# Performance work log

Measured on AMD Instinct MI355X. Metric: run time of the kernel, lower is better.

The kernel has to match this reference:

```python
import jax, jax.numpy as jnp
import numpy as np

B, N, DIM = 4, 1024, 1024
H, DH, ORDER = 16, 64, 3
MAXREL = 64
INNER = H * DH
VOCAB = 2 * MAXREL + 1
SCALE = DH ** -0.5
TOPK = int(0.25 * N)  # topk_ratio=0.25 default when top_k is None


def setup_inputs() -> dict:
    key = jax.random.key(0)
    ks = jax.random.split(key, 8)
    s = 0.02
    return {
        "x": jax.random.normal(ks[0], (B, N, DIM), jnp.float32),
        "Wqkv": jax.random.normal(ks[1], (3 * INNER, DIM), jnp.float32) * s,
        "bqkv": jnp.zeros((3 * INNER,), jnp.float32),
        "Wout": jax.random.normal(ks[2], (DIM, INNER), jnp.float32) * s,
        "bout": jnp.zeros((DIM,), jnp.float32),
        "rel_k_emb": jax.random.normal(ks[3], (VOCAB, DH), jnp.float32) * s,
        "rel_v_emb": jax.random.normal(ks[4], (VOCAB, DH), jnp.float32) * s,
        "alphas_raw": jax.random.normal(ks[5], (ORDER, H), jnp.float32) * 0.5,
    }


def reference(x, Wqkv, bqkv, Wout, bout, rel_k_emb, rel_v_emb, alphas_raw):
    b, n, _ = x.shape
    qkv = x @ Wqkv.T + bqkv  # [b, n, 3*inner]
    q, k, v = jnp.split(qkv, 3, axis=-1)
    to_heads = lambda t: t.reshape(b, n, H, DH).transpose(0, 2, 1, 3)  # b h n d
    q, k, v = to_heads(q), to_heads(k), to_heads(v)

    scores = jnp.einsum('bhid,bhjd->bhij', q, k) * SCALE

    # relative position bias on keys
    coords = jnp.arange(n)
    dist = jnp.clip(coords[:, None] - coords[None, :], -MAXREL, MAXREL) + MAXREL  # [n, n]
    rel_k = rel_k_emb[dist]  # [n, n, d]
    scores = scores + jnp.einsum('bhid,ijd->bhij', q, rel_k)

    # top-k thresholding per query row
    top_vals = jax.lax.top_k(scores, TOPK)[0]
    threshold = top_vals[..., -1:]
    scores = jnp.where(scores < threshold, -jnp.inf, scores)

    attn = jax.nn.softmax(scores, axis=-1)  # [b, h, n, n]

    rel_v = rel_v_emb[dist]  # [n, n, d]
    alphas = jax.nn.sigmoid(alphas_raw)  # [order, h]

    # monomial-basis polynomial filter: res = sum_i alpha_i * A^(i+1) V (+ relV term at i=0)
    res = jnp.zeros_like(v)
    v_curr = v
    for i in range(ORDER):
        a_v = jnp.einsum('bhij,bhjd->bhid', attn, v_curr)
        if i == 0:
            a_v = a_v + jnp.einsum('bhij,ijd->bhid', attn, rel_v)
        v_curr = a_v
        res = res + alphas[i][None, :, None, None] * v_curr

    out = res.transpose(0, 2, 1, 3).reshape(b, n, INNER)
    return out @ Wout.T + bout
```

## Files before the change

kernel.cpp:

```cpp
#include <hip/hip_runtime.h>

typedef unsigned short u16;
typedef unsigned int   u32;
typedef unsigned long long u64;
typedef __bf16 bf16x8 __attribute__((ext_vector_type(8)));
typedef float  floatx4 __attribute__((ext_vector_type(4)));

#define DEV static __device__ __forceinline__

DEV u16 f2bf(float f){ u32 x = __float_as_uint(f); return (u16)((x + 0x7fffu + ((x>>16)&1u)) >> 16); }
DEV float bf2f(u16 h){ return __uint_as_float(((u32)h)<<16); }
DEV u32 cvt_pk_bf16(float a, float b){ u32 r; asm("v_cvt_pk_bf16_f32 %0, %1, %2" : "=v"(r) : "v"(a), "v"(b)); return r; }

DEV void load_lds16(const u16* g, u16* l){
  __builtin_amdgcn_global_load_lds((const __attribute__((address_space(1))) u32*)g,
                                   (__attribute__((address_space(3))) u32*)l, 16, 0, 0);
}

template<int BM, int BN, int MODE>
__global__ __launch_bounds__(256) void gemm_bt(
    const u16* __restrict__ A, const u16* __restrict__ Bm, float* __restrict__ C,
    const float* __restrict__ bias, int K, int lda, int ldb, int ldc, int ncmax,
    long long sA, long long sB, long long sC,
    u16* __restrict__ vout, float* __restrict__ resb, const float* __restrict__ araw,
    int order, int accum)
{
  constexpr int BK = 32;
  constexpr int MT = BM/32;
  constexpr int NT = (BN/2)/16;
  __shared__ u16 smem[8704];
  u16* As = smem;
  u16* Bs = smem + BM*BK;

  const int tid = threadIdx.x, wid = tid>>6, lane = tid&63;
  const int z = blockIdx.z;
  const int m0 = blockIdx.y * BM, n0 = blockIdx.x * BN;
  const u16* Ab = A + (long long)z*sA;
  const u16* Bb = Bm + (long long)z*sB;

  const int srow = tid>>2, schunk = (tid&3)*8;
  const u16* ga0 = Ab + (long long)(m0 + srow)*lda + schunk;
  const u16* gb0 = Bb + (long long)(n0 + srow)*ldb + schunk;
  const u16* ga1 = (BM==128) ? Ab + (long long)(m0 + 64 + srow)*lda + schunk : nullptr;
  const u16* gb1 = (BN==128) ? Bb + (long long)(n0 + 64 + srow)*ldb + schunk : nullptr;

  u16* lA0 = As + (wid*16)*BK;
  u16* lA1 = As + (64 + wid*16)*BK;
  u16* lB0 = Bs + (wid*16)*BK;
  u16* lB1 = Bs + (64 + wid*16)*BK;

  const int wm = wid>>1, wn = wid&1;
  const int lr = lane&15, lk = (lane>>4)*8, lq = lane>>4;

  floatx4 acc[MT][NT] = {};

  for (int k = 0; k < K; k += BK) {
    __syncthreads();
    load_lds16(ga0 + k, lA0);
    if constexpr (BM == 128) load_lds16(ga1 + k, lA1);
    load_lds16(gb0 + k, lB0);
    if constexpr (BN == 128) load_lds16(gb1 + k, lB1);
    __syncthreads();
    bf16x8 af[MT];
#pragma unroll
    for (int mt=0; mt<MT; ++mt)
      af[mt] = *(const bf16x8*)(As + (wm*(BM/2) + mt*16 + lr)*BK + lk);
#pragma unroll
    for (int nt=0; nt<NT; ++nt) {
      bf16x8 bfr = *(const bf16x8*)(Bs + (wn*(BN/2) + nt*16 + lr)*BK + lk);
#pragma unroll
      for (int mt=0; mt<MT; ++mt)
        acc[mt][nt] = __builtin_amdgcn_mfma_f32_16x16x32_bf16(af[mt], bfr, acc[mt][nt], 0, 0, 0);
    }
  }

  if constexpr (MODE == 0) {
    float* Cb = C + (long long)z*sC;
#pragma unroll
    for (int nt=0; nt<NT; ++nt) {
      const int col = n0 + wn*(BN/2) + nt*16 + lr;
      if (col < ncmax) {
        const float bv = bias ? bias[col] : 0.f;
#pragma unroll
        for (int mt=0; mt<MT; ++mt) {
#pragma unroll
          for (int r=0; r<4; ++r) {
            const int row = m0 + wm*(BM/2) + mt*16 + lq*4 + r;
            Cb[(long long)row*ldc + col] = acc[mt][nt][r] + bv;
          }
        }
      }
    }
  } else {
    const int h = z & 15;
    const float alpha = 1.f/(1.f + __expf(-araw[order*16 + h]));
    float* rb = resb + (long long)z * 65536;
    __syncthreads();
#pragma unroll
    for (int nt=0; nt<NT; ++nt) {
      const int d = wn*32 + nt*16 + lr;
#pragma unroll
      for (int mt=0; mt<MT; ++mt) {
#pragma unroll
        for (int r=0; r<4; ++r) {
          const int row = wm*(BM/2) + mt*16 + lq*4 + r;
          const float v = acc[mt][nt][r];
          const long long ri = (long long)(m0+row)*64 + d;
          rb[ri] = accum ? (rb[ri] + alpha*v) : (alpha*v);
          smem[d*136 + row] = f2bf(v);
        }
      }
    }
    __syncthreads();
    const int dd = tid>>2, cc = (tid&3)*(BM/4);
    u16* vp = vout + (long long)z*75776 + (long long)dd*1184 + m0 + cc;
    const u16* sp = smem + dd*136 + cc;
#pragma unroll
    for (int j=0; j<BM/4; j+=8) {
      uint4 uu;
      uu.x = sp[j+0] | ((u32)sp[j+1]<<16);
      uu.y = sp[j+2] | ((u32)sp[j+3]<<16);
      uu.z = sp[j+4] | ((u32)sp[j+5]<<16);
      uu.w = sp[j+6] | ((u32)sp[j+7]<<16);
      *(uint4*)(vp + j) = uu;
    }
  }
}

__global__ __launch_bounds__(1024, 8) void score_topk(
    const u16* __restrict__ qF,
    const u16* __restrict__ kxF,
    u16* __restrict__ P)
{
  constexpr int SROW = 1156;
  __shared__ float sm[16*SROW];
  const int tid = threadIdx.x, wid = tid>>6, lane = tid&63;
  const int L = blockIdx.x;
  const int z  = (L & 7) + ((L >> 9) << 3);
  const int mt = (L >> 3) & 63;
  const int m0 = mt*16;
  const int lr = lane&15, lq = lane>>4;

  const u16* Aq = qF + (((long long)z*64 + mt)*6*64 + lane)*8;
  const u16* Bq = kxF + ((long long)z*80*6*64 + lane)*8;

  bf16x8 af[6];
#pragma unroll
  for (int kc=0;kc<6;++kc) af[kc] = *(const bf16x8*)(Aq + kc*512);

  const int base = wid*5;
  {
    floatx4 acc[5];
#pragma unroll
    for (int t=0;t<5;++t) acc[t] = floatx4{0.f,0.f,0.f,0.f};
#pragma unroll
    for (int t=0;t<5;++t){
      if (base + t < 73){
        const u16* bp = Bq + (long long)(base+t)*3072;
        bf16x8 b0 = *(const bf16x8*)(bp);
        bf16x8 b1 = *(const bf16x8*)(bp + 512);
        bf16x8 b2 = *(const bf16x8*)(bp + 1024);
        bf16x8 b3 = *(const bf16x8*)(bp + 1536);
        bf16x8 b4 = *(const bf16x8*)(bp + 2048);
        bf16x8 b5 = *(const bf16x8*)(bp + 2560);
        acc[t] = __builtin_amdgcn_mfma_f32_16x16x32_bf16(af[0], b0, acc[t], 0, 0, 0);
        acc[t] = __builtin_amdgcn_mfma_f32_16x16x32_bf16(af[1], b1, acc[t], 0, 0, 0);
        acc[t] = __builtin_amdgcn_mfma_f32_16x16x32_bf16(af[2], b2, acc[t], 0, 0, 0);
        acc[t] = __builtin_amdgcn_mfma_f32_16x16x32_bf16(af[3], b3, acc[t], 0, 0, 0);
        acc[t] = __builtin_amdgcn_mfma_f32_16x16x32_bf16(af[4], b4, acc[t], 0, 0, 0);
        acc[t] = __builtin_amdgcn_mfma_f32_16x16x32_bf16(af[5], b5, acc[t], 0, 0, 0);
      }
    }
#pragma unroll
    for (int t=0;t<5;++t){
      if (base + t < 73){
        const int col = (base+t)*16 + lr;
        if (col < 1153){
#pragma unroll
          for (int r=0;r<4;++r) sm[(lq*4+r)*SROW + col] = acc[t][r];
        }
      }
    }
  }
  __syncthreads();

  {
    const int row = wid;
    const int i = m0 + row;
    float* R = sm + row*SROW;

    float v[16];
#pragma unroll
    for (int x=0;x<8;++x){
      float2 f = *(const float2*)(R + x*128 + lane*2);
      v[2*x] = f.x; v[2*x+1] = f.y;
    }
#pragma unroll
    for (int x=0;x<16;++x){
      const int j = (x>>1)*128 + lane*2 + (x&1);
      int dl = i - j; dl = dl > 64 ? 64 : (dl < -64 ? -64 : dl);
      v[x] += R[1024 + dl + 64];
    }
    u32 u[16];
#pragma unroll
    for (int x=0;x<16;++x){
      u32 bb = __float_as_uint(v[x]);
      u[x] = bb ^ ((u32)((int)bb >> 31) | 0x80000000u);
    }
    u32 thr = 0;
#pragma unroll 1
    for (int bit=31; bit>=0; --bit){
      const u32 cand = thr | (1u<<bit);
      int c = 0;
#pragma unroll
      for (int x=0;x<16;++x) c += __popcll(__ballot(u[x] >= cand));
      if (c == 256){
        u32 mn = 0xFFFFFFFFu;
#pragma unroll
        for (int x=0;x<16;++x) if (u[x] >= cand && u[x] < mn) mn = u[x];
        for (int o=32;o;o>>=1){ u32 t = __shfl_xor(mn, o); mn = t < mn ? t : mn; }
        thr = mn;
        break;
      }
      if (c > 256) thr = cand;
    }
    float m = -3.0e38f;
#pragma unroll
    for (int x=0;x<16;++x) m = fmaxf(m, v[x]);
    for (int o=32;o;o>>=1) m = fmaxf(m, __shfl_xor(m, o));
    float e[16]; float Z = 0.f;
#pragma unroll
    for (int x=0;x<16;++x){
      e[x] = (u[x] >= thr) ? __expf(v[x]-m) : 0.f;
      Z += e[x];
    }
    for (int o=32;o;o>>=1) Z += __shfl_xor(Z, o);
    const float rz = 1.f / Z;

    u16* Pr = P + ((long long)z*1024 + i)*1184;
    u32* Pr32 = (u32*)Pr;
    float s0 = 0.f, s1 = 0.f;
#pragma unroll
    for (int x=0;x<8;++x){
      const float p0 = e[2*x]*rz, p1 = e[2*x+1]*rz;
      *(float2*)(R + x*128 + lane*2) = float2{p0, p1};
      Pr32[x*64 + lane] = cvt_pk_bf16(p0, p1);
      const int j0 = x*128 + lane*2;
      if (j0     >= i+64) s0 += p0;
      if (j0     <= i-64) s1 += p0;
      if (j0 + 1 >= i+64) s0 += p1;
      if (j0 + 1 <= i-64) s1 += p1;
    }
    for (int o=32;o;o>>=1){ s0 += __shfl_xor(s0,o); s1 += __shfl_xor(s1,o); }
    {
      const int t = lane + 1;
      const int j = i + 64 - t;
      const float wv = (j>=0 && j<1024) ? R[j] : 0.f;
      Pr[1024 + t] = f2bf(wv);
      if (lane < 63){
        const int t2 = lane + 65;
        const int j2 = i + 64 - t2;
        const float wv2 = (j2>=0 && j2<1024) ? R[j2] : 0.f;
        Pr[1024 + t2] = f2bf(wv2);
      }
      if (lane == 0){ Pr[1024] = f2bf(s0); Pr[1152] = f2bf(s1); }
      if (lane >= 33) Pr[1120 + lane] = 0;
    }
  }
}

__global__ __launch_bounds__(256) void planeize(const float* __restrict__ src, u16* __restrict__ dst,
                                                int total, int modeB){
  int idx = blockIdx.x*256 + threadIdx.x;
  if (idx >= total) return;
  int c = idx & 1023, r = idx >> 10;
  float v = src[idx];
  u16 hi = f2bf(v); u16 lo = f2bf(v - bf2f(hi));
  u16* d = dst + (long long)r*3072 + c;
  if (modeB){ d[0]=hi; d[1024]=hi; d[2048]=lo; }
  else      { d[0]=hi; d[1024]=lo; d[2048]=hi; }
}

__global__ __launch_bounds__(256) void build_qk(const float* __restrict__ qkv,
                                                u16* __restrict__ qF, u16* __restrict__ kxF){
  int idx = blockIdx.x*256 + threadIdx.x;
  int d = idx & 63, n = (idx>>6) & 1023, bh = idx >> 16;
  int b = bh >> 4, h = bh & 15;
  long long src = (long long)(b*1024 + n)*3072 + h*64 + d;
  float qv = qkv[src];
  float kv = qkv[src + 1024] * 0.125f;
  u16 qhi=f2bf(qv), qlo=f2bf(qv - bf2f(qhi));
  u16 khi=f2bf(kv), klo=f2bf(kv - bf2f(khi));
  const int lane = (n&15) + (((d&31)>>3)<<4);
  const int elem = d&7, kc0 = d>>5;
  u16* q = qF + ((((long long)bh*64 + (n>>4))*6*64) + lane)*8 + elem;
  q[(kc0+0)*512] = qhi; q[(kc0+2)*512] = qlo; q[(kc0+4)*512] = qhi;
  u16* kx = kxF + ((((long long)bh*80 + (n>>4))*6*64) + lane)*8 + elem;
  kx[(kc0+0)*512] = khi; kx[(kc0+2)*512] = khi; kx[(kc0+4)*512] = klo;
}

__global__ __launch_bounds__(256) void build_kxrel(const float* __restrict__ relk, u16* __restrict__ kxF){
  int idx = blockIdx.x*256 + threadIdx.x;
  int d = idx & 63, t = (idx>>6) & 255, bh = idx >> 14;
  u16 hi=0, lo=0;
  if (t < 129){ float v = relk[t*64 + d]; hi = f2bf(v); lo = f2bf(v - bf2f(hi)); }
  const int nrow = 1024 + t;
  const int lane = (t&15) + (((d&31)>>3)<<4);
  const int elem = d&7, kc0 = d>>5;
  u16* kx = kxF + ((((long long)bh*80 + (nrow>>4))*6*64) + lane)*8 + elem;
  kx[(kc0+0)*512] = hi; kx[(kc0+2)*512] = hi; kx[(kc0+4)*512] = lo;
}

__global__ __launch_bounds__(256) void build_vT(const float* __restrict__ qkv, u16* __restrict__ vA){
  __shared__ float tb[64][65];
  int bh = blockIdx.x >> 4, ntile = blockIdx.x & 15;
  int b = bh >> 4, h = bh & 15;
  int tid = threadIdx.x;
  int nl = tid >> 2, dc = (tid & 3)*16;
  const float* sp = qkv + (long long)(b*1024 + ntile*64 + nl)*3072 + 2048 + h*64 + dc;
#pragma unroll
  for (int j=0;j<16;j+=4){
    float4 f = *(const float4*)(sp + j);
    tb[dc+j+0][nl]=f.x; tb[dc+j+1][nl]=f.y; tb[dc+j+2][nl]=f.z; tb[dc+j+3][nl]=f.w;
  }
  __syncthreads();
  int d = tid >> 2, nc = (tid & 3)*16;
  u16* dp = vA + ((long long)bh*64 + d)*1184 + ntile*64 + nc;
#pragma unroll
  for (int j=0;j<16;j+=8){
    u16 a0=f2bf(tb[d][nc+j+0]), a1=f2bf(tb[d][nc+j+1]), a2=f2bf(tb[d][nc+j+2]), a3=f2bf(tb[d][nc+j+3]);
    u16 a4=f2bf(tb[d][nc+j+4]), a5=f2bf(tb[d][nc+j+5]), a6=f2bf(tb[d][nc+j+6]), a7=f2bf(tb[d][nc+j+7]);
    uint4 uu; uu.x=a0|((u32)a1<<16); uu.y=a2|((u32)a3<<16); uu.z=a4|((u32)a5<<16); uu.w=a6|((u32)a7<<16);
    *(uint4*)(dp + j) = uu;
  }
}

__global__ __launch_bounds__(256) void build_vText(const float* __restrict__ relv, u16* __restrict__ vA){
  int idx = blockIdx.x*256 + threadIdx.x;
  int t = idx % 160; int rest = idx / 160; int d = rest & 63; int bh = rest >> 6;
  u16 hv = 0;
  if (t < 129) hv = f2bf(relv[t*64 + d]);
  vA[((long long)bh*64 + d)*1184 + 1024 + t] = hv;
}

__global__ __launch_bounds__(256) void build_resS(const float* __restrict__ res, u16* __restrict__ resS){
  int idx = blockIdx.x*256 + threadIdx.x;
  int d = idx & 63, n = (idx>>6) & 1023, bh = idx >> 16;
  int b = bh >> 4, h = bh & 15;
  float v = res[idx];
  u16 hi = f2bf(v), lo = f2bf(v - bf2f(hi));
  u16* p = resS + (long long)(b*1024 + n)*3072 + h*64 + d;
  p[0]=hi; p[1024]=lo; p[2048]=hi;
}

extern "C" void kernel_launch(void* const* d_in, const int* in_sizes, int n_in,
                              void* d_out, int out_size, void* d_ws, size_t ws_size,
                              hipStream_t stream) {
  const float* x    = (const float*)d_in[0];
  const float* Wqkv = (const float*)d_in[1];
  const float* bqkv = (const float*)d_in[2];
  const float* Wout = (const float*)d_in[3];
  const float* bout = (const float*)d_in[4];
  const float* relk = (const float*)d_in[5];
  const float* relv = (const float*)d_in[6];
  const float* araw = (const float*)d_in[7];
  float* out = (float*)d_out;

  char* w = (char*)d_ws;
  size_t off = 0;
  auto take = [&](size_t bytes)->char*{ char* p = w + off; off += (bytes + 255) & ~(size_t)255; return p; };

  char* regionA = take(94371840);
  u16*   xS    = (u16*)  (regionA);
  u16*   wqS   = (u16*)  (regionA + 25165824);
  float* qkv32 = (float*)(regionA + 44040192);
  u16*   Ph    = (u16*)  (regionA);
  u16*   resS  = (u16*)  (regionA);
  u16*   woS   = (u16*)  (regionA + 25165824);
  u16*   qF    = (u16*)take(25165824);
  u16*   kxF   = (u16*)take(31457280);
  u16*   vA    = (u16*)take(9699328);
  u16*   vB    = (u16*)take(9699328);
  float* res   = (float*)take(16777216);
  (void)ws_size; (void)in_sizes; (void)n_in; (void)out_size;

  planeize<<<16384,256,0,stream>>>(x,    xS,  4194304, 0);
  planeize<<<12288,256,0,stream>>>(Wqkv, wqS, 3145728, 1);
  gemm_bt<128,128,0><<<dim3(16,32,1),256,0,stream>>>(xS, wqS, qkv32, bqkv,
      3072, 3072, 3072, 3072, 2048, 0, 0, 0, nullptr, nullptr, nullptr, 0, 0);
  gemm_bt<128,128,0><<<dim3(8,32,1),256,0,stream>>>(xS, wqS + (long long)2048*3072,
      qkv32 + 2048, bqkv + 2048,
      1024, 3072, 3072, 3072, 1024, 0, 0, 0, nullptr, nullptr, nullptr, 0, 0);
  build_qk   <<<16384,256,0,stream>>>(qkv32, qF, kxF);
  build_kxrel<<<4096, 256,0,stream>>>(relk, kxF);
  build_vT   <<<1024, 256,0,stream>>>(qkv32, vA);
  build_vText<<<2560, 256,0,stream>>>(relv, vA);

  for (int half = 0; half < 2; ++half) {
    const long long zo = (long long)half * 32;
    score_topk<<<2048,1024,0,stream>>>(qF + zo*196608, kxF + zo*245760, Ph);
    gemm_bt<64,64,1><<<dim3(1,16,32),256,0,stream>>>(Ph, vA + zo*75776, nullptr, nullptr,
        1184, 1184, 1184, 0, 0, 1212416LL, 75776LL, 0LL,
        vB + zo*75776, res + zo*65536, araw, 0, 0);
    gemm_bt<64,64,1><<<dim3(1,16,32),256,0,stream>>>(Ph, vB + zo*75776, nullptr, nullptr,
        1024, 1184, 1184, 0, 0, 1212416LL, 75776LL, 0LL,
        vA + zo*75776, res + zo*65536, araw, 1, 1);
    gemm_bt<64,64,1><<<dim3(1,16,32),256,0,stream>>>(Ph, vA + zo*75776, nullptr, nullptr,
        1024, 1184, 1184, 0, 0, 1212416LL, 75776LL, 0LL,
        vB + zo*75776, res + zo*65536, araw, 2, 1);
  }

  build_resS<<<16384,256,0,stream>>>(res, resS);
  planeize  <<<4096, 256,0,stream>>>(Wout, woS, 1048576, 1);
  gemm_bt<64,128,0><<<dim3(8,64,1),256,0,stream>>>(resS, woS, out, bout,
      3072, 3072, 3072, 1024, 1024, 0, 0, 0, nullptr, nullptr, nullptr, 0, 0);
}
```

Measured before the change: 617.6 us.

## Swizzle GEMM LDS layout and add small-tile double-buffered AV kernel

Applies an XOR swizzle to the LDS tile layout in gemm_bt, with a matching permuted global-load mapping, to cut bank conflicts on fragment reads. It also replaces the 64x64 attention-times-V GEMM launches with a new av16 kernel that uses 16-row tiles, double-buffered LDS staging and 2048 blocks to raise occupancy and parallelism. The last hop skips writing V back since nothing reads it. The smaller tiles reload the V tile for every 16 query rows, trading data reuse for parallelism.

New measurement: 630.9 us. 2.2% more time.

```diff
diff --git a/kernel.cpp b/kernel.cpp
--- a/kernel.cpp
+++ b/kernel.cpp
@@ -15,6 +15,18 @@
 DEV void load_lds16(const u16* g, u16* l){
   __builtin_amdgcn_global_load_lds((const __attribute__((address_space(1))) u32*)g,
                                    (__attribute__((address_space(3))) u32*)l, 16, 0, 0);
+}
+
+DEV u32 unswz64(u32 p){
+  u32 r0 = ((p>>6) ^ (p>>8)) & 1u;
+  u32 b4 = ((p>>4) & 1u) ^ r0;
+  u32 b5 = ((p>>5) ^ (p>>7)) & 1u;
+  return (p & ~0x70u) | (b4<<4) | (b5<<5) | (r0<<6);
+}
+DEV bf16x8 ldfrag(const u16* base, int row, int lane){
+  u32 off = ((u32)row<<6) + (((u32)lane>>4)<<4);
+  off ^= (u32)(row&7)<<4;
+  return *(const bf16x8*)((const char*)base + off);
 }
 
 template<int BM, int BN, int MODE>
@@ -38,7 +50,8 @@
   const u16* Ab = A + (long long)z*sA;
   const u16* Bb = Bm + (long long)z*sB;
 
-  const int srow = tid>>2, schunk = (tid&3)*8;
+  const u32 g = unswz64((u32)tid*16);
+  const int srow = g>>6, schunk = (g&63)>>1;
   const u16* ga0 = Ab + (long long)(m0 + srow)*lda + schunk;
   const u16* gb0 = Bb + (long long)(n0 + srow)*ldb + schunk;
   const u16* ga1 = (BM==128) ? Ab + (long long)(m0 + 64 + srow)*lda + schunk : nullptr;
@@ -50,7 +63,7 @@
   u16* lB1 = Bs + (64 + wid*16)*BK;
 
   const int wm = wid>>1, wn = wid&1;
-  const int lr = lane&15, lk = (lane>>4)*8, lq = lane>>4;
+  const int lr = lane&15, lq = lane>>4;
 
   floatx4 acc[MT][NT] = {};
 
@@ -64,10 +77,10 @@
     bf16x8 af[MT];
 #pragma unroll
     for (int mt=0; mt<MT; ++mt)
-      af[mt] = *(const bf16x8*)(As + (wm*(BM/2) + mt*16 + lr)*BK + lk);
+      af[mt] = ldfrag(As, wm*(BM/2) + mt*16 + lr, lane);
 #pragma unroll
     for (int nt=0; nt<NT; ++nt) {
-      bf16x8 bfr = *(const bf16x8*)(Bs + (wn*(BN/2) + nt*16 + lr)*BK + lk);
+      bf16x8 bfr = ldfrag(Bs, wn*(BN/2) + nt*16 + lr, lane);
 #pragma unroll
       for (int mt=0; mt<MT; ++mt)
         acc[mt][nt] = __builtin_amdgcn_mfma_f32_16x16x32_bf16(af[mt], bfr, acc[mt][nt], 0, 0, 0);
@@ -124,6 +137,66 @@
       uu.w = sp[j+6] | ((u32)sp[j+7]<<16);
       *(uint4*)(vp + j) = uu;
     }
+  }
+}
+
+__global__ __launch_bounds__(256, 8) void av16(
+    const u16* __restrict__ P,
+    const u16* __restrict__ V,
+    u16* __restrict__ vout,
+    float* __restrict__ resb,
+    const float* __restrict__ araw, int K, int order, int accum, int wv)
+{
+  __shared__ u16 As[2][16*32];
+  __shared__ u16 Bs[2][64*32];
+  const int tid = threadIdx.x, wid = tid>>6, lane = tid&63;
+  const int L = blockIdx.x;
+  const int z = (L & 7) + ((L >> 9) << 3);
+  const int m0 = ((L >> 3) & 63) * 16;
+  const int lr = lane&15, lq = lane>>4;
+
+  const u32 ga = unswz64((u32)lane*16);
+  const int arow = ga>>6, acolu = (ga&63)>>1;
+  const u32 gb = unswz64((u32)tid*16);
+  const int brow = gb>>6, bcolu = (gb&63)>>1;
+  const u16* srcA = P + (long long)z*1212416 + (long long)(m0 + arow)*1184 + acolu;
+  const u16* srcB = V + (long long)z*75776  + (long long)brow*1184 + bcolu;
+
+  auto stage = [&](int buf, int k){
+    if (wid == 0) load_lds16(srcA + k, &As[buf][lane*8]);
+    load_lds16(srcB + k, &Bs[buf][tid*8]);
+  };
+
+  stage(0, 0);
+  __syncthreads();
+
+  floatx4 acc = {0.f,0.f,0.f,0.f};
+  const int nk = K >> 5;
+  for (int s = 0; s < nk; ++s){
+    const int cur = s & 1;
+    if (s + 1 < nk) stage(cur ^ 1, (s+1) << 5);
+    bf16x8 a = ldfrag(As[cur], lr, lane);
+    bf16x8 b = ldfrag(Bs[cur], wid*16 + lr, lane);
+    acc = __builtin_amdgcn_mfma_f32_16x16x32_bf16(a, b, acc, 0, 0, 0);
+    __syncthreads();
+  }
+
+  const int h = z & 15;
+  const float alpha = 1.f/(1.f + __expf(-araw[order*16 + h]));
+  const int d = wid*16 + lr;
+  float* rb = resb + (long long)z * 65536;
+  u32 w0, w1;
+#pragma unroll
+  for (int r=0; r<4; ++r){
+    const float v = acc[r];
+    const long long ri = (long long)(m0 + lq*4 + r)*64 + d;
+    rb[ri] = accum ? (rb[ri] + alpha*v) : (alpha*v);
+  }
+  if (wv){
+    w0 = f2bf(acc[0]) | ((u32)f2bf(acc[1])<<16);
+    w1 = f2bf(acc[2]) | ((u32)f2bf(acc[3])<<16);
+    u16* vp = vout + (long long)z*75776 + (long long)d*1184 + m0 + lq*4;
+    *(uint2*)vp = uint2{w0, w1};
   }
 }
 
@@ -399,15 +472,12 @@
   for (int half = 0; half < 2; ++half) {
     const long long zo = (long long)half * 32;
     score_topk<<<2048,1024,0,stream>>>(qF + zo*196608, kxF + zo*245760, Ph);
-    gemm_bt<64,64,1><<<dim3(1,16,32),256,0,stream>>>(Ph, vA + zo*75776, nullptr, nullptr,
-        1184, 1184, 1184, 0, 0, 1212416LL, 75776LL, 0LL,
-        vB + zo*75776, res + zo*65536, araw, 0, 0);
-    gemm_bt<64,64,1><<<dim3(1,16,32),256,0,stream>>>(Ph, vB + zo*75776, nullptr, nullptr,
-        1024, 1184, 1184, 0, 0, 1212416LL, 75776LL, 0LL,
-        vA + zo*75776, res + zo*65536, araw, 1, 1);
-    gemm_bt<64,64,1><<<dim3(1,16,32),256,0,stream>>>(Ph, vA + zo*75776, nullptr, nullptr,
-        1024, 1184, 1184, 0, 0, 1212416LL, 75776LL, 0LL,
-        vB + zo*75776, res + zo*65536, araw, 2, 1);
+    av16<<<2048,256,0,stream>>>(Ph, vA + zo*75776, vB + zo*75776, res + zo*65536,
+        araw, 1184, 0, 0, 1);
+    av16<<<2048,256,0,stream>>>(Ph, vB + zo*75776, vA + zo*75776, res + zo*65536,
+        araw, 1024, 1, 1, 1);
+    av16<<<2048,256,0,stream>>>(Ph, vA + zo*75776, vB + zo*75776, res + zo*65536,
+        araw, 1024, 2, 1, 0);
   }
 
   build_resS<<<16384,256,0,stream>>>(res, resS);
```

## Swizzle GEMM LDS tiles and use 8-wave kernel for projection GEMMs

Applied to the files above, without the earlier changes.

Adds an XOR swizzle to the LDS tile layout. The global source address of each lane's global_load_lds is permuted, and fragment reads apply the matching XOR, to cut LDS bank conflicts in the bf16 MFMA GEMMs. The batched P·V gemm_bt loses its 128-row second-load path, since it is now used only with 64x64 tiles. A new 512-thread, 8-wave gemm8 kernel replaces gemm_bt for the QKV and output projections, so each wave holds fewer accumulators and more waves share each staged tile. The risk is higher register and LDS pressure per block, and the swizzle math must stay consistent between the write and read sides.

Measured after the change: 596.4 us. 3.4% less time.

```diff
diff --git a/kernel.cpp b/kernel.cpp
--- a/kernel.cpp
+++ b/kernel.cpp
@@ -15,6 +15,18 @@
 DEV void load_lds16(const u16* g, u16* l){
   __builtin_amdgcn_global_load_lds((const __attribute__((address_space(1))) u32*)g,
                                    (__attribute__((address_space(3))) u32*)l, 16, 0, 0);
+}
+
+DEV u32 unswz64(u32 p){
+  u32 r0 = ((p>>6) ^ (p>>8)) & 1u;
+  u32 b4 = ((p>>4) & 1u) ^ r0;
+  u32 b5 = ((p>>5) ^ (p>>7)) & 1u;
+  return (p & ~0x70u) | (b4<<4) | (b5<<5) | (r0<<6);
+}
+DEV bf16x8 ldfrag(const u16* base, int row, int lane){
+  u32 off = ((u32)row<<6) + (((u32)lane>>4)<<4);
+  off ^= (u32)(row&7)<<4;
+  return *(const bf16x8*)((const char*)base + off);
 }
 
 template<int BM, int BN, int MODE>
@@ -38,36 +50,31 @@
   const u16* Ab = A + (long long)z*sA;
   const u16* Bb = Bm + (long long)z*sB;
 
-  const int srow = tid>>2, schunk = (tid&3)*8;
+  const u32 g = unswz64((u32)tid*16);
+  const int srow = g>>6, schunk = (g&63)>>1;
   const u16* ga0 = Ab + (long long)(m0 + srow)*lda + schunk;
   const u16* gb0 = Bb + (long long)(n0 + srow)*ldb + schunk;
-  const u16* ga1 = (BM==128) ? Ab + (long long)(m0 + 64 + srow)*lda + schunk : nullptr;
-  const u16* gb1 = (BN==128) ? Bb + (long long)(n0 + 64 + srow)*ldb + schunk : nullptr;
 
   u16* lA0 = As + (wid*16)*BK;
-  u16* lA1 = As + (64 + wid*16)*BK;
   u16* lB0 = Bs + (wid*16)*BK;
-  u16* lB1 = Bs + (64 + wid*16)*BK;
 
   const int wm = wid>>1, wn = wid&1;
-  const int lr = lane&15, lk = (lane>>4)*8, lq = lane>>4;
+  const int lr = lane&15, lq = lane>>4;
 
   floatx4 acc[MT][NT] = {};
 
   for (int k = 0; k < K; k += BK) {
     __syncthreads();
     load_lds16(ga0 + k, lA0);
-    if constexpr (BM == 128) load_lds16(ga1 + k, lA1);
     load_lds16(gb0 + k, lB0);
-    if constexpr (BN == 128) load_lds16(gb1 + k, lB1);
     __syncthreads();
     bf16x8 af[MT];
 #pragma unroll
     for (int mt=0; mt<MT; ++mt)
-      af[mt] = *(const bf16x8*)(As + (wm*(BM/2) + mt*16 + lr)*BK + lk);
+      af[mt] = ldfrag(As, wm*(BM/2) + mt*16 + lr, lane);
 #pragma unroll
     for (int nt=0; nt<NT; ++nt) {
-      bf16x8 bfr = *(const bf16x8*)(Bs + (wn*(BN/2) + nt*16 + lr)*BK + lk);
+      bf16x8 bfr = ldfrag(Bs, wn*(BN/2) + nt*16 + lr, lane);
 #pragma unroll
       for (int mt=0; mt<MT; ++mt)
         acc[mt][nt] = __builtin_amdgcn_mfma_f32_16x16x32_bf16(af[mt], bfr, acc[mt][nt], 0, 0, 0);
@@ -123,6 +130,67 @@
       uu.z = sp[j+4] | ((u32)sp[j+5]<<16);
       uu.w = sp[j+6] | ((u32)sp[j+7]<<16);
       *(uint4*)(vp + j) = uu;
+    }
+  }
+}
+
+template<int BM, int BN>
+__global__ __launch_bounds__(512, 4) void gemm8(
+    const u16* __restrict__ A, const u16* __restrict__ Bm, float* __restrict__ C,
+    const float* __restrict__ bias, int K, int lda, int ldb, int ldc, int ncmax)
+{
+  constexpr int MT = (BM/2)/16;
+  constexpr int NT = (BN/4)/16;
+  __shared__ u16 As[BM*32];
+  __shared__ u16 Bs[BN*32];
+
+  const int tid = threadIdx.x, wid = tid>>6, lane = tid&63;
+  const int m0 = blockIdx.y * BM, n0 = blockIdx.x * BN;
+
+  const u32 g = unswz64((u32)tid*16);
+  const int srow = g>>6, schunk = (g&63)>>1;
+  const u16* ga0 = A  + (long long)(m0 + srow)*lda + schunk;
+  const u16* gb0 = Bm + (long long)(n0 + srow)*ldb + schunk;
+
+  u16* lA = As + (wid<<9);
+  u16* lB = Bs + (wid<<9);
+
+  const int wm = wid>>2, wn = wid&3;
+  const int lr = lane&15, lq = lane>>4;
+
+  floatx4 acc[MT][NT] = {};
+
+  for (int k = 0; k < K; k += 32) {
+    __syncthreads();
+    if (BM == 128 || wid < 4) load_lds16(ga0 + k, lA);
+    load_lds16(gb0 + k, lB);
+    __syncthreads();
+    bf16x8 af[MT];
+#pragma unroll
+    for (int mt=0; mt<MT; ++mt)
+      af[mt] = ldfrag(As, wm*(BM/2) + mt*16 + lr, lane);
+#pragma unroll
+    for (int nt=0; nt<NT; ++nt) {
+      bf16x8 bfr = ldfrag(Bs, wn*(BN/4) + nt*16 + lr, lane);
+#pragma unroll
+      for (int mt=0; mt<MT; ++mt)
+        acc[mt][nt] = __builtin_amdgcn_mfma_f32_16x16x32_bf16(af[mt], bfr, acc[mt][nt], 0, 0, 0);
+    }
+  }
+
+#pragma unroll
+  for (int nt=0; nt<NT; ++nt) {
+    const int col = n0 + wn*(BN/4) + nt*16 + lr;
+    if (col < ncmax) {
+      const float bv = bias ? bias[col] : 0.f;
+#pragma unroll
+      for (int mt=0; mt<MT; ++mt) {
+#pragma unroll
+        for (int r=0; r<4; ++r) {
+          const int row = m0 + wm*(BM/2) + mt*16 + lq*4 + r;
+          C[(long long)row*ldc + col] = acc[mt][nt][r] + bv;
+        }
+      }
     }
   }
 }
@@ -386,11 +454,10 @@
 
   planeize<<<16384,256,0,stream>>>(x,    xS,  4194304, 0);
   planeize<<<12288,256,0,stream>>>(Wqkv, wqS, 3145728, 1);
-  gemm_bt<128,128,0><<<dim3(16,32,1),256,0,stream>>>(xS, wqS, qkv32, bqkv,
-      3072, 3072, 3072, 3072, 2048, 0, 0, 0, nullptr, nullptr, nullptr, 0, 0);
-  gemm_bt<128,128,0><<<dim3(8,32,1),256,0,stream>>>(xS, wqS + (long long)2048*3072,
-      qkv32 + 2048, bqkv + 2048,
-      1024, 3072, 3072, 3072, 1024, 0, 0, 0, nullptr, nullptr, nullptr, 0, 0);
+  gemm8<128,128><<<dim3(16,32,1),512,0,stream>>>(xS, wqS, qkv32, bqkv,
+      3072, 3072, 3072, 3072, 2048);
+  gemm8<128,128><<<dim3(8,32,1),512,0,stream>>>(xS, wqS + (long long)2048*3072,
+      qkv32 + 2048, bqkv + 2048, 1024, 3072, 3072, 3072, 1024);
   build_qk   <<<16384,256,0,stream>>>(qkv32, qF, kxF);
   build_kxrel<<<4096, 256,0,stream>>>(relk, kxF);
   build_vT   <<<1024, 256,0,stream>>>(qkv32, vA);
@@ -412,6 +479,6 @@
 
   build_resS<<<16384,256,0,stream>>>(res, resS);
   planeize  <<<4096, 256,0,stream>>>(Wout, woS, 1048576, 1);
-  gemm_bt<64,128,0><<<dim3(8,64,1),256,0,stream>>>(resS, woS, out, bout,
-      3072, 3072, 3072, 1024, 1024, 0, 0, 0, nullptr, nullptr, nullptr, 0, 0);
-}
+  gemm8<64,128><<<dim3(8,64,1),512,0,stream>>>(resS, woS, out, bout,
+      3072, 3072, 3072, 1024, 1024);
+}
```
